# Kernel optimization log

Hardware: AMD Instinct MI355X
Metric: run time of the kernel (lower is better)

The kernel has to match this reference:

```python
import jax, jax.numpy as jnp
import numpy as np

# Uniform 3-level taxonomy: 128 roots, branching 16 then 16.
N0, B1, B2 = 128, 16, 16
N1, N2 = N0 * B1, N0 * B1 * B2          # 2048, 32768
TOTAL = N0 + N1 + N2                    # 34944
BATCH = 1024
W = (1.0, 1.0, 1.0)                     # level_weights
NEG = -100000000.0                      # fill value used by the torch module


def _ce(logits, tgt):
    # per-sample cross entropy, reduction='none': logits [B,C], tgt [B] -> [B]
    return -jnp.take_along_axis(jax.nn.log_softmax(logits, axis=-1), tgt[:, None], axis=1)[:, 0]


def setup_inputs() -> dict:
    key = jax.random.key(0)
    k1, k2, k3, k4 = jax.random.split(key, 4)
    outputs = jax.random.normal(k1, (BATCH, TOTAL), dtype=jnp.float32)
    # hierarchically consistent labels (relative-within-level ids, as labelmap expects)
    r0 = jax.random.randint(k2, (BATCH,), 0, N0, dtype=jnp.int32)
    r1 = jax.random.randint(k3, (BATCH,), 0, B1, dtype=jnp.int32)
    r2 = jax.random.randint(k4, (BATCH,), 0, B2, dtype=jnp.int32)
    lab1 = r0 * B1 + r1
    lab2 = lab1 * B2 + r2
    level_labels = jnp.stack([r0, lab1, lab2], axis=1)  # [B, 3] int32
    return {"outputs": outputs, "level_labels": level_labels}


def reference(outputs, level_labels):
    lab0, lab1, lab2 = level_labels[:, 0], level_labels[:, 1], level_labels[:, 2]
    r1 = lab1 - lab0 * B1   # new_level_labels[1]: label relative to true parent's children
    r2 = lab2 - lab1 * B2   # new_level_labels[2]

    out0 = outputs[:, :N0]                 # [B, N0]
    out1 = outputs[:, N0:N0 + N1]          # [B, N1]
    out2 = outputs[:, N0 + N1:]            # [B, N2]

    # ---- level 0: possible children == all roots, so masked CE == full CE
    loss0 = _ce(out0, lab0)
    pred0 = jnp.argmax(out0, axis=1).astype(jnp.int32)          # predicted root (relative)
    found0 = pred0 != lab0                                      # found_incorrect after level 0

    # ---- level 1
    g1_true = jnp.take_along_axis(out1.reshape(BATCH, N0, B1), lab0[:, None, None], axis=1)[:, 0, :]
    loss1 = jnp.where(found0, _ce(out1, lab1), _ce(g1_true, r1))
    g1_pred = jnp.take_along_axis(out1.reshape(BATCH, N0, B1), pred0[:, None, None], axis=1)[:, 0, :]
    pred1_in = jnp.argmax(g1_pred, axis=1).astype(jnp.int32)    # argmax within predicted parent's children
    pred1 = pred0 * B1 + pred1_in                               # predicted level-1 class (relative)
    found1 = found0 | (pred1_in != r1)

    # ---- level 2
    g2_true = jnp.take_along_axis(out2.reshape(BATCH, N1, B2), lab1[:, None, None], axis=1)[:, 0, :]
    loss2 = jnp.where(found1, _ce(out2, lab2), _ce(g2_true, r2))

    # ---- outputs_new: level-0 slice fully copied; levels 1/2 only children of the predicted path
    mask1 = (jnp.arange(N1, dtype=jnp.int32) // B1)[None, :] == pred0[:, None]
    mask2 = (jnp.arange(N2, dtype=jnp.int32) // B2)[None, :] == pred1[:, None]
    outputs_new = jnp.concatenate(
        [out0, jnp.where(mask1, out1, NEG), jnp.where(mask2, out2, NEG)], axis=1)

    # torch accumulates size-1 tensors; torch.mean of the final [1] tensor == total sum
    loss = jnp.sum(W[0] * loss0 + W[1] * loss1 + W[2] * loss2)
    return outputs_new, loss
```

## Files before the change

### kernel.cpp

```cpp
#include <hip/hip_runtime.h>
#include <math.h>

#define N0v 128
#define B1v 16
#define B2v 16
#define N1v 2048
#define N2v 32768
#define TOTALv 34944
#define BATCHv 1024
#define NEGV -100000000.0f

typedef __attribute__((ext_vector_type(4))) float f32x4;

__global__ __launch_bounds__(1024, 8) void row_kernel(
    const float* __restrict__ outs, const int* __restrict__ labels,
    float* __restrict__ out, float* __restrict__ partials)
{
    const int b   = blockIdx.x;
    const int tid = threadIdx.x;
    const int wid = tid >> 6, lane = tid & 63;
    const float* rowp = outs + (size_t)b * TOTALv;
    float*       orow = out  + (size_t)b * TOTALv;
    const f32x4* rv4 = reinterpret_cast<const f32x4*>(rowp);
    f32x4*       ov4 = reinterpret_cast<f32x4*>(orow);
    const f32x4  neg4 = {NEGV, NEGV, NEGV, NEGV};

    __shared__ float sm_gsum[128];
    __shared__ int   sm_gidx[128];
    __shared__ float s_wmax[2]; __shared__ int s_wmi[2];
    __shared__ float s_red[16][3];
    __shared__ int   s_i[2];

    const int lab0 = labels[b * 3 + 0];
    const int lab1 = labels[b * 3 + 1];
    const int lab2 = labels[b * 3 + 2];

    float v0 = 0.f;
    if (tid < N0v) v0 = rowp[tid];
    f32x4 a = {0.f, 0.f, 0.f, 0.f};
    if (tid < 512) a = rv4[32 + tid];
    const f32x4* b2 = rv4 + 544;
    f32x4*       o2 = ov4 + 544;
    const f32x4 x0 = b2[tid];
    const f32x4 x1 = b2[tid + 1024];
    const f32x4 x2 = b2[tid + 2048];
    const f32x4 x3 = b2[tid + 3072];
    const f32x4 x4 = b2[tid + 4096];
    const f32x4 x5 = b2[tid + 5120];
    const f32x4 x6 = b2[tid + 6144];
    const f32x4 x7 = b2[tid + 7168];
    float eg2 = 0.f;
    if (tid < 16) eg2 = rowp[N0v + N1v + lab1 * B2v + tid];
    float t0 = 0.f, t1 = 0.f, t2 = 0.f;
    if (tid == 0) { t0 = rowp[lab0]; t1 = rowp[N0v + lab1]; t2 = rowp[N0v + N1v + lab2]; }
    __builtin_amdgcn_sched_barrier(0);

    float s1 = 0.f;
    if (tid < 512) {
        s1 = __expf(a.x) + __expf(a.y) + __expf(a.z) + __expf(a.w);
        float gm = a.x; int gi = 0;
        if (a.y > gm) { gm = a.y; gi = 1; }
        if (a.z > gm) { gm = a.z; gi = 2; }
        if (a.w > gm) { gm = a.w; gi = 3; }
        gi += (tid & 3) * 4;
        float gs = s1;
        float ov = __shfl_xor(gm, 1); int oi = __shfl_xor(gi, 1);
        gs += __shfl_xor(gs, 1);
        if (ov > gm || (ov == gm && oi < gi)) { gm = ov; gi = oi; }
        ov = __shfl_xor(gm, 2); oi = __shfl_xor(gi, 2);
        gs += __shfl_xor(gs, 2);
        if (ov > gm || (ov == gm && oi < gi)) { gm = ov; gi = oi; }
        if ((tid & 3) == 0) { sm_gsum[tid >> 2] = gs; sm_gidx[tid >> 2] = gi; }
    }

    if (tid < N0v) {
        float mv = v0; int mi = tid;
        #pragma unroll
        for (int off = 32; off; off >>= 1) {
            float ovv = __shfl_down(mv, off);
            int   oii = __shfl_down(mi, off);
            if (ovv > mv || (ovv == mv && oii < mi)) { mv = ovv; mi = oii; }
        }
        if (lane == 0) { s_wmax[wid] = mv; s_wmi[wid] = mi; }
    }

    if (tid < 16) {
        eg2 = __expf(eg2);
        #pragma unroll
        for (int off = 8; off; off >>= 1) eg2 += __shfl_xor(eg2, off);
    }

    float s2 = 0.f;
    s2 += __expf(x0.x)+__expf(x0.y)+__expf(x0.z)+__expf(x0.w);
    s2 += __expf(x1.x)+__expf(x1.y)+__expf(x1.z)+__expf(x1.w);
    s2 += __expf(x2.x)+__expf(x2.y)+__expf(x2.z)+__expf(x2.w);
    s2 += __expf(x3.x)+__expf(x3.y)+__expf(x3.z)+__expf(x3.w);
    s2 += __expf(x4.x)+__expf(x4.y)+__expf(x4.z)+__expf(x4.w);
    s2 += __expf(x5.x)+__expf(x5.y)+__expf(x5.z)+__expf(x5.w);
    s2 += __expf(x6.x)+__expf(x6.y)+__expf(x6.z)+__expf(x6.w);
    s2 += __expf(x7.x)+__expf(x7.y)+__expf(x7.z)+__expf(x7.w);

    float r0 = (tid < N0v) ? __expf(v0) : 0.f;
    #pragma unroll
    for (int off = 32; off; off >>= 1) {
        r0 += __shfl_down(r0, off);
        s1 += __shfl_down(s1, off);
        s2 += __shfl_down(s2, off);
    }
    if (lane == 0) { s_red[wid][0] = r0; s_red[wid][1] = s1; s_red[wid][2] = s2; }

    __syncthreads();

    if (tid == 0) {
        float m0 = s_wmax[0]; int p0 = s_wmi[0];
        if (s_wmax[1] > m0 || (s_wmax[1] == m0 && s_wmi[1] < p0)) { m0 = s_wmax[1]; p0 = s_wmi[1]; }
        const int p1i = sm_gidx[p0];
        s_i[0] = p0; s_i[1] = p1i;
        float S0 = 0.f, S1 = 0.f, S2 = 0.f;
        #pragma unroll
        for (int w = 0; w < 16; ++w) { S0 += s_red[w][0]; S1 += s_red[w][1]; S2 += s_red[w][2]; }
        const float Sg1 = sm_gsum[lab0];
        const int r1 = lab1 - lab0 * B1v;
        const bool found0 = (p0 != lab0);
        const bool found1 = found0 || (p1i != r1);
        const float loss0 = __logf(S0) - t0;
        const float loss1 = (found0 ? __logf(S1) : __logf(Sg1)) - t1;
        const float loss2 = (found1 ? __logf(S2) : __logf(eg2)) - t2;
        partials[b] = loss0 + loss1 + loss2;
    }

    __syncthreads();
    const int pred0 = s_i[0];
    const int pred1 = pred0 * B1v + s_i[1];

    if (tid < 512) {
        __builtin_nontemporal_store(((tid >> 2) == pred0) ? a : neg4, &ov4[32 + tid]);
        if (tid < N0v) __builtin_nontemporal_store(v0, &orow[tid]);
    }
    __builtin_nontemporal_store(((tid         >> 2) == pred1) ? x0 : neg4, &o2[tid]);
    __builtin_nontemporal_store((((tid + 1024) >> 2) == pred1) ? x1 : neg4, &o2[tid + 1024]);
    __builtin_nontemporal_store((((tid + 2048) >> 2) == pred1) ? x2 : neg4, &o2[tid + 2048]);
    __builtin_nontemporal_store((((tid + 3072) >> 2) == pred1) ? x3 : neg4, &o2[tid + 3072]);
    __builtin_nontemporal_store((((tid + 4096) >> 2) == pred1) ? x4 : neg4, &o2[tid + 4096]);
    __builtin_nontemporal_store((((tid + 5120) >> 2) == pred1) ? x5 : neg4, &o2[tid + 5120]);
    __builtin_nontemporal_store((((tid + 6144) >> 2) == pred1) ? x6 : neg4, &o2[tid + 6144]);
    __builtin_nontemporal_store((((tid + 7168) >> 2) == pred1) ? x7 : neg4, &o2[tid + 7168]);
}

__global__ __launch_bounds__(256) void loss_reduce(
    const float* __restrict__ partials, float* __restrict__ out_loss)
{
    __shared__ float sh[4];
    const int tid = threadIdx.x;
    float s = 0.f;
    for (int i = tid; i < BATCHv; i += 256) s += partials[i];
    #pragma unroll
    for (int off = 32; off; off >>= 1) s += __shfl_down(s, off);
    if ((tid & 63) == 0) sh[tid >> 6] = s;
    __syncthreads();
    if (tid == 0) *out_loss = sh[0] + sh[1] + sh[2] + sh[3];
}

extern "C" void kernel_launch(void* const* d_in, const int* in_sizes, int n_in,
                              void* d_out, int out_size, void* d_ws, size_t ws_size,
                              hipStream_t stream) {
    const float* outs   = (const float*)d_in[0];
    const int*   labels = (const int*)d_in[1];
    float*       out    = (float*)d_out;
    float*       part   = (float*)d_ws;

    row_kernel<<<BATCHv, 1024, 0, stream>>>(outs, labels, out, part);
    loss_reduce<<<1, 256, 0, stream>>>(part, out + (size_t)BATCHv * TOTALv);
}
```

Measured before the change: 54.12 us.

## Stream level-2 row through a rolling prefetch loop, deferring its exp-sum

Instead of holding all eight level-2 vectors in registers before the reductions, the kernel now keeps one vector live and prefetches the next inside a loop, computing the exp-sum and storing masked output as it goes. The level-2 sum reduction moves after the predicted-path broadcast, and a third block barrier finalizes the loss. This cuts register pressure and lets stores overlap with loads, at the cost of exposing load latency one step at a time and an extra synchronization.

After: 50.71 us. 6.3% less time.

```diff
diff --git a/kernel.cpp b/kernel.cpp
--- a/kernel.cpp
+++ b/kernel.cpp
@@ -30,6 +30,7 @@
     __shared__ float s_wmax[2]; __shared__ int s_wmi[2];
     __shared__ float s_red[16][3];
     __shared__ int   s_i[2];
+    __shared__ float s_loss[2];
 
     const int lab0 = labels[b * 3 + 0];
     const int lab1 = labels[b * 3 + 1];
@@ -41,14 +42,7 @@
     if (tid < 512) a = rv4[32 + tid];
     const f32x4* b2 = rv4 + 544;
     f32x4*       o2 = ov4 + 544;
-    const f32x4 x0 = b2[tid];
-    const f32x4 x1 = b2[tid + 1024];
-    const f32x4 x2 = b2[tid + 2048];
-    const f32x4 x3 = b2[tid + 3072];
-    const f32x4 x4 = b2[tid + 4096];
-    const f32x4 x5 = b2[tid + 5120];
-    const f32x4 x6 = b2[tid + 6144];
-    const f32x4 x7 = b2[tid + 7168];
+    f32x4 cur = b2[tid];
     float eg2 = 0.f;
     if (tid < 16) eg2 = rowp[N0v + N1v + lab1 * B2v + tid];
     float t0 = 0.f, t1 = 0.f, t2 = 0.f;
@@ -90,24 +84,13 @@
         for (int off = 8; off; off >>= 1) eg2 += __shfl_xor(eg2, off);
     }
 
-    float s2 = 0.f;
-    s2 += __expf(x0.x)+__expf(x0.y)+__expf(x0.z)+__expf(x0.w);
-    s2 += __expf(x1.x)+__expf(x1.y)+__expf(x1.z)+__expf(x1.w);
-    s2 += __expf(x2.x)+__expf(x2.y)+__expf(x2.z)+__expf(x2.w);
-    s2 += __expf(x3.x)+__expf(x3.y)+__expf(x3.z)+__expf(x3.w);
-    s2 += __expf(x4.x)+__expf(x4.y)+__expf(x4.z)+__expf(x4.w);
-    s2 += __expf(x5.x)+__expf(x5.y)+__expf(x5.z)+__expf(x5.w);
-    s2 += __expf(x6.x)+__expf(x6.y)+__expf(x6.z)+__expf(x6.w);
-    s2 += __expf(x7.x)+__expf(x7.y)+__expf(x7.z)+__expf(x7.w);
-
     float r0 = (tid < N0v) ? __expf(v0) : 0.f;
     #pragma unroll
     for (int off = 32; off; off >>= 1) {
         r0 += __shfl_down(r0, off);
         s1 += __shfl_down(s1, off);
-        s2 += __shfl_down(s2, off);
     }
-    if (lane == 0) { s_red[wid][0] = r0; s_red[wid][1] = s1; s_red[wid][2] = s2; }
+    if (lane == 0) { s_red[wid][0] = r0; s_red[wid][1] = s1; }
 
     __syncthreads();
 
@@ -116,17 +99,17 @@
         if (s_wmax[1] > m0 || (s_wmax[1] == m0 && s_wmi[1] < p0)) { m0 = s_wmax[1]; p0 = s_wmi[1]; }
         const int p1i = sm_gidx[p0];
         s_i[0] = p0; s_i[1] = p1i;
-        float S0 = 0.f, S1 = 0.f, S2 = 0.f;
+        float S0 = 0.f, S1 = 0.f;
         #pragma unroll
-        for (int w = 0; w < 16; ++w) { S0 += s_red[w][0]; S1 += s_red[w][1]; S2 += s_red[w][2]; }
+        for (int w = 0; w < 16; ++w) { S0 += s_red[w][0]; S1 += s_red[w][1]; }
         const float Sg1 = sm_gsum[lab0];
         const int r1 = lab1 - lab0 * B1v;
         const bool found0 = (p0 != lab0);
         const bool found1 = found0 || (p1i != r1);
         const float loss0 = __logf(S0) - t0;
         const float loss1 = (found0 ? __logf(S1) : __logf(Sg1)) - t1;
-        const float loss2 = (found1 ? __logf(S2) : __logf(eg2)) - t2;
-        partials[b] = loss0 + loss1 + loss2;
+        s_loss[0] = loss0 + loss1 - t2 + (found1 ? 0.f : __logf(eg2));
+        s_loss[1] = found1 ? 1.f : 0.f;
     }
 
     __syncthreads();
@@ -137,14 +120,29 @@
         __builtin_nontemporal_store(((tid >> 2) == pred0) ? a : neg4, &ov4[32 + tid]);
         if (tid < N0v) __builtin_nontemporal_store(v0, &orow[tid]);
     }
-    __builtin_nontemporal_store(((tid         >> 2) == pred1) ? x0 : neg4, &o2[tid]);
-    __builtin_nontemporal_store((((tid + 1024) >> 2) == pred1) ? x1 : neg4, &o2[tid + 1024]);
-    __builtin_nontemporal_store((((tid + 2048) >> 2) == pred1) ? x2 : neg4, &o2[tid + 2048]);
-    __builtin_nontemporal_store((((tid + 3072) >> 2) == pred1) ? x3 : neg4, &o2[tid + 3072]);
-    __builtin_nontemporal_store((((tid + 4096) >> 2) == pred1) ? x4 : neg4, &o2[tid + 4096]);
-    __builtin_nontemporal_store((((tid + 5120) >> 2) == pred1) ? x5 : neg4, &o2[tid + 5120]);
-    __builtin_nontemporal_store((((tid + 6144) >> 2) == pred1) ? x6 : neg4, &o2[tid + 6144]);
-    __builtin_nontemporal_store((((tid + 7168) >> 2) == pred1) ? x7 : neg4, &o2[tid + 7168]);
+
+    float s2 = 0.f;
+    int idx = tid;
+    #pragma unroll
+    for (int it = 0; it < 7; ++it) {
+        const f32x4 nxt = b2[idx + 1024];
+        s2 += __expf(cur.x) + __expf(cur.y) + __expf(cur.z) + __expf(cur.w);
+        __builtin_nontemporal_store(((idx >> 2) == pred1) ? cur : neg4, &o2[idx]);
+        cur = nxt; idx += 1024;
+    }
+    s2 += __expf(cur.x) + __expf(cur.y) + __expf(cur.z) + __expf(cur.w);
+    __builtin_nontemporal_store(((idx >> 2) == pred1) ? cur : neg4, &o2[idx]);
+
+    #pragma unroll
+    for (int off = 32; off; off >>= 1) s2 += __shfl_down(s2, off);
+    if (lane == 0) s_red[wid][2] = s2;
+    __syncthreads();
+    if (tid == 0) {
+        float S2 = 0.f;
+        #pragma unroll
+        for (int w = 0; w < 16; ++w) S2 += s_red[w][2];
+        partials[b] = s_loss[0] + s_loss[1] * __logf(S2);
+    }
 }
 
 __global__ __launch_bounds__(256) void loss_reduce(
```
